# Kernel tuning notes

Hardware: AMD Instinct MI355X
Metric: run time of the kernel (lower is better)

Reference implementation:

```python
import jax, jax.numpy as jnp
import numpy as np

B, L, T = 16, 256, 256
ENC, DEC, MEL, SPK = 256, 1024, 80, 256
ATT, FILT, K = 128, 32, 31


def setup_inputs() -> dict:
    key = jax.random.key(0)
    ks = jax.random.split(key, 32)
    s = 0.05
    r = lambda k, shape: jax.random.normal(k, shape, dtype=jnp.float32) * s
    return {
        'encoder_outputs': jax.random.normal(ks[0], (B, L, ENC), dtype=jnp.float32),
        'speaker_embed': jax.random.normal(ks[1], (B, SPK), dtype=jnp.float32),
        'mels': jax.random.normal(ks[2], (B, T, MEL), dtype=jnp.float32),
        # prenet
        'W_pre1': r(ks[3], (DEC, MEL)), 'b_pre1': jnp.zeros((DEC,), jnp.float32),
        'W_pre2': r(ks[4], (DEC, DEC)), 'b_pre2': jnp.zeros((DEC,), jnp.float32),
        # speaker projection
        'W_sp': r(ks[5], (DEC, SPK)), 'b_sp': jnp.zeros((DEC,), jnp.float32),
        # location-sensitive attention (Tacotron-2 style)
        'W_q': r(ks[6], (ATT, DEC)),
        'W_m': r(ks[7], (ATT, ENC)),
        'W_loc_conv': r(ks[8], (FILT, 2, K)),
        'W_loc': r(ks[9], (ATT, FILT)),
        'v_att': r(ks[10], (ATT,)),
        # LSTM cells
        'W_ih1': r(ks[11], (4 * DEC, DEC + ENC)), 'W_hh1': r(ks[12], (4 * DEC, DEC)),
        'b_ih1': jnp.zeros((4 * DEC,), jnp.float32), 'b_hh1': jnp.zeros((4 * DEC,), jnp.float32),
        'W_ih2': r(ks[13], (4 * DEC, DEC)), 'W_hh2': r(ks[14], (4 * DEC, DEC)),
        'b_ih2': jnp.zeros((4 * DEC,), jnp.float32), 'b_hh2': jnp.zeros((4 * DEC,), jnp.float32),
        # output projections
        'W_mel': r(ks[15], (MEL, DEC)), 'b_mel': jnp.zeros((MEL,), jnp.float32),
        'W_stop': r(ks[16], (1, DEC)), 'b_stop': jnp.zeros((1,), jnp.float32),
    }


def _lstm_cell(x, h, c, W_ih, W_hh, b_ih, b_hh):
    g = x @ W_ih.T + h @ W_hh.T + b_ih + b_hh
    i, f, gg, o = jnp.split(g, 4, axis=-1)
    c2 = jax.nn.sigmoid(f) * c + jax.nn.sigmoid(i) * jnp.tanh(gg)
    h2 = jax.nn.sigmoid(o) * jnp.tanh(c2)
    return h2, c2


def reference(encoder_outputs, speaker_embed, mels,
              W_pre1, b_pre1, W_pre2, b_pre2, W_sp, b_sp,
              W_q, W_m, W_loc_conv, W_loc, v_att,
              W_ih1, W_hh1, b_ih1, b_hh1, W_ih2, W_hh2, b_ih2, b_hh2,
              W_mel, b_mel, W_stop, b_stop):
    b = encoder_outputs.shape[0]
    proc_mem = jnp.einsum('bld,ad->bla', encoder_outputs, W_m)  # [B,L,ATT]
    spk = speaker_embed @ W_sp.T + b_sp                          # [B,DEC]
    # teacher forcing: step 0 uses zeros, step i>0 uses mels[:, i] (matches torch loop)
    prev_mel_seq = jnp.concatenate([jnp.zeros_like(mels[:, :1]), mels[:, 1:]], axis=1)
    prev_mel_seq = prev_mel_seq.transpose(1, 0, 2)               # [T,B,MEL]

    def step(carry, prev_mel):
        h1, c1, h2, c2, prev_w, cum_w = carry
        # prenet (dropout = identity in eval)
        p = jax.nn.relu(prev_mel @ W_pre1.T + b_pre1)
        p = jax.nn.relu(p @ W_pre2.T + b_pre2)
        q = p + spk
        # location features over [prev, cumulative] attention weights
        loc = jnp.stack([prev_w, cum_w], axis=1)                 # [B,2,L]
        f = jax.lax.conv_general_dilated(loc, W_loc_conv, (1,), [(K // 2, K // 2)],
                                         dimension_numbers=('NCH', 'OIH', 'NCH'))  # [B,FILT,L]
        e = jnp.einsum('bla,a->bl', jnp.tanh((q @ W_q.T)[:, None, :]
                                             + jnp.einsum('bcl,ac->bla', f, W_loc)
                                             + proc_mem), v_att)  # [B,L]
        w = jax.nn.softmax(e, axis=1)
        ctx = jnp.einsum('bl,bld->bd', w, encoder_outputs)        # [B,ENC]
        h1n, c1n = _lstm_cell(jnp.concatenate([p, ctx], axis=1), h1, c1, W_ih1, W_hh1, b_ih1, b_hh1)
        h2n, c2n = _lstm_cell(h1n, h2, c2, W_ih2, W_hh2, b_ih2, b_hh2)
        mel = h2n @ W_mel.T + b_mel
        stop = jax.nn.sigmoid(h2n @ W_stop.T + b_stop)
        return (h1n, c1n, h2n, c2n, w, cum_w + w), (mel, stop)

    z = lambda d: jnp.zeros((b, d), jnp.float32)
    carry0 = (z(DEC), z(DEC), z(DEC), z(DEC), z(L), z(L))
    _, (mel_seq, stop_seq) = jax.lax.scan(step, carry0, prev_mel_seq)
    return mel_seq.transpose(1, 0, 2), stop_seq.transpose(1, 0, 2)
```

## Files before the change

kernel.cpp:

```cpp
#include <hip/hip_runtime.h>


namespace {

constexpr int TT = 256, BB = 16, LL = 256, MELD = 80, FILTD = 32, KC = 31;
constexpr int P1 = 2308;
constexpr int P2 = 2052;

typedef float f32x4 __attribute__((ext_vector_type(4)));

struct Args {
  const float *enc, *spe, *mels;
  const float *Wpre1, *bpre1, *Wpre2, *bpre2, *Wsp, *bsp;
  const float *Wq, *Wm, *Wconv, *Wloc, *vatt;
  const float *Wih1, *Whh1, *bih1, *bhh1;
  const float *Wih2, *Whh2, *bih2, *bhh2;
  const float *Wmel, *bmel, *Wstop, *bstop;
  float *p, *X, *qp2, *pm2, *prevmel;
  float *h1a, *h1b, *c1, *h2a, *h2b, *c2;
  float *cum, *wexp, *uctx, *pctx, *psum, *spkvec, *spkq;
  float *W81, *b81, *tmp;
  int *slots, *epoch, *pslots, *pepoch;
  float *out;
};

__device__ __forceinline__ float fast_tanh(float x) {
  float ax = fabsf(x);
  float e = __expf(-2.f * ax);
  float t = (1.f - e) / (1.f + e);
  return copysignf(t, x);
}
__device__ __forceinline__ float fast_sig(float x) { return 1.f / (1.f + __expf(-x)); }

__device__ __forceinline__ float cld1(const float* p) {
  float v;
  asm volatile("global_load_dword %0, %1, off sc0 sc1\n\ts_waitcnt vmcnt(0)"
               : "=v"(v) : "v"(p) : "memory");
  return v;
}
__device__ __forceinline__ int cldi(const int* p) {
  int v;
  asm volatile("global_load_dword %0, %1, off sc0 sc1\n\ts_waitcnt vmcnt(0)"
               : "=v"(v) : "v"(p) : "memory");
  return v;
}
__device__ __forceinline__ void cst1(float* p, float v) {
  asm volatile("global_store_dword %0, %1, off sc0 sc1" :: "v"(p), "v"(v) : "memory");
}
__device__ __forceinline__ void csti(int* p, int v) {
  asm volatile("global_store_dword %0, %1, off sc0 sc1" :: "v"(p), "v"(v) : "memory");
}
__device__ __forceinline__ void cld4(f32x4 d[4], const f32x4* q0, const f32x4* q1,
                                     const f32x4* q2, const f32x4* q3) {
  asm volatile(
      "global_load_dwordx4 %0, %4, off sc0 sc1\n\t"
      "global_load_dwordx4 %1, %5, off sc0 sc1\n\t"
      "global_load_dwordx4 %2, %6, off sc0 sc1\n\t"
      "global_load_dwordx4 %3, %7, off sc0 sc1\n\t"
      "s_waitcnt vmcnt(0)"
      : "=&v"(d[0]), "=&v"(d[1]), "=&v"(d[2]), "=&v"(d[3])
      : "v"(q0), "v"(q1), "v"(q2), "v"(q3)
      : "memory");
}
__device__ __forceinline__ void cld8(f32x4 d[8], const f32x4* q0, const f32x4* q1,
                                     const f32x4* q2, const f32x4* q3, const f32x4* q4,
                                     const f32x4* q5, const f32x4* q6, const f32x4* q7) {
  asm volatile(
      "global_load_dwordx4 %0, %8, off sc0 sc1\n\t"
      "global_load_dwordx4 %1, %9, off sc0 sc1\n\t"
      "global_load_dwordx4 %2, %10, off sc0 sc1\n\t"
      "global_load_dwordx4 %3, %11, off sc0 sc1\n\t"
      "global_load_dwordx4 %4, %12, off sc0 sc1\n\t"
      "global_load_dwordx4 %5, %13, off sc0 sc1\n\t"
      "global_load_dwordx4 %6, %14, off sc0 sc1\n\t"
      "global_load_dwordx4 %7, %15, off sc0 sc1\n\t"
      "s_waitcnt vmcnt(0)"
      : "=&v"(d[0]), "=&v"(d[1]), "=&v"(d[2]), "=&v"(d[3]),
        "=&v"(d[4]), "=&v"(d[5]), "=&v"(d[6]), "=&v"(d[7])
      : "v"(q0), "v"(q1), "v"(q2), "v"(q3), "v"(q4), "v"(q5), "v"(q6), "v"(q7)
      : "memory");
}
__device__ __forceinline__ void cld8d(float d[8], const float* q0, const float* q1,
                                      const float* q2, const float* q3, const float* q4,
                                      const float* q5, const float* q6, const float* q7) {
  asm volatile(
      "global_load_dword %0, %8, off sc0 sc1\n\t"
      "global_load_dword %1, %9, off sc0 sc1\n\t"
      "global_load_dword %2, %10, off sc0 sc1\n\t"
      "global_load_dword %3, %11, off sc0 sc1\n\t"
      "global_load_dword %4, %12, off sc0 sc1\n\t"
      "global_load_dword %5, %13, off sc0 sc1\n\t"
      "global_load_dword %6, %14, off sc0 sc1\n\t"
      "global_load_dword %7, %15, off sc0 sc1\n\t"
      "s_waitcnt vmcnt(0)"
      : "=&v"(d[0]), "=&v"(d[1]), "=&v"(d[2]), "=&v"(d[3]),
        "=&v"(d[4]), "=&v"(d[5]), "=&v"(d[6]), "=&v"(d[7])
      : "v"(q0), "v"(q1), "v"(q2), "v"(q3), "v"(q4), "v"(q5), "v"(q6), "v"(q7)
      : "memory");
}

__device__ __forceinline__ void gridbar(int* slots, int* epoch, int target) {
  __syncthreads();
  if (blockIdx.x == 0) {
    if (threadIdx.x == 0) csti(&slots[0], target);
    while (cldi(&slots[threadIdx.x * 32]) < target) __builtin_amdgcn_s_sleep(1);
    __syncthreads();
    if (threadIdx.x == 0) csti(epoch, target);
  } else {
    if (threadIdx.x == 0) {
      csti(&slots[blockIdx.x * 32], target);
      while (cldi(epoch) < target) __builtin_amdgcn_s_sleep(8);
    }
  }
  __syncthreads();
}

__global__ void k_init(float* base, int n) {
  int i = blockIdx.x * blockDim.x + threadIdx.x;
  if (i < n) base[i] = 0.f;
}

__global__ void k_setpsum(float* psum) {
  if (threadIdx.x < 16) psum[256 + threadIdx.x * 16] = 1.f;
}

__global__ void k_prevmel(Args a) {
  int i = blockIdx.x * blockDim.x + threadIdx.x;
  if (i >= TT * BB * MELD) return;
  int m = i % MELD;
  int tb = i / MELD;
  int b = tb & 15, t = tb >> 4;
  a.prevmel[i] = (t == 0) ? 0.f : a.mels[(b * TT + t) * MELD + m];
}

__global__ void k_spkvec(Args a) {
  int i = blockIdx.x * blockDim.x + threadIdx.x;
  if (i >= BB * 1024) return;
  int b = i >> 10, j = i & 1023;
  const float* x = a.spe + b * 256;
  const float* w = a.Wsp + j * 256;
  float s = a.bsp[j];
  for (int k = 0; k < 256; ++k) s += x[k] * w[k];
  a.spkvec[i] = s;
}

__global__ void k_spkq(Args a) {
  int i = blockIdx.x * blockDim.x + threadIdx.x;
  if (i >= BB * 128) return;
  int b = i >> 7, q = i & 127;
  const float* x = a.spkvec + b * 1024;
  const float* w = a.Wq + q * 1024;
  float s = 0.f;
  for (int k = 0; k < 1024; ++k) s += x[k] * w[k];
  a.spkq[i] = s;
}

__global__ void k_prep81(Args a) {
  int i = blockIdx.x * blockDim.x + threadIdx.x;
  if (i < 81 * 1024) {
    int r = i >> 10, k = i & 1023;
    a.W81[i] = (r < 80) ? a.Wmel[r * 1024 + k] : a.Wstop[k];
  }
  if (i < 81) a.b81[i] = (i < 80) ? a.bmel[i] : a.bstop[0];
}

__global__ __launch_bounds__(256) void k_gemm(const float* __restrict__ A,
                                              const float* __restrict__ Bm,
                                              const float* __restrict__ bias,
                                              float* __restrict__ C,
                                              int M, int N, int K, int act) {
  __shared__ __align__(16) float As[16][132];
  __shared__ __align__(16) float Bs[16][68];
  const int bm = blockIdx.y * 128, bn = blockIdx.x * 64;
  const int tid = threadIdx.x;
  const int tm = (tid >> 4) * 8, tn = (tid & 15) * 4;
  float acc[8][4] = {};
  for (int k0 = 0; k0 < K; k0 += 16) {
    for (int i = tid; i < 512; i += 256) {
      int m = i >> 2, kq = i & 3;
      float4 v = *(const float4*)(A + (size_t)(bm + m) * K + k0 + kq * 4);
      As[kq * 4 + 0][m] = v.x; As[kq * 4 + 1][m] = v.y;
      As[kq * 4 + 2][m] = v.z; As[kq * 4 + 3][m] = v.w;
    }
    {
      int m = tid >> 2, kq = tid & 3;
      float4 v = *(const float4*)(Bm + (size_t)(bn + m) * K + k0 + kq * 4);
      Bs[kq * 4 + 0][m] = v.x; Bs[kq * 4 + 1][m] = v.y;
      Bs[kq * 4 + 2][m] = v.z; Bs[kq * 4 + 3][m] = v.w;
    }
    __syncthreads();
#pragma unroll
    for (int kk = 0; kk < 16; ++kk) {
      float4 a0 = *(const float4*)&As[kk][tm];
      float4 a1 = *(const float4*)&As[kk][tm + 4];
      float4 b0 = *(const float4*)&Bs[kk][tn];
      float av[8] = {a0.x, a0.y, a0.z, a0.w, a1.x, a1.y, a1.z, a1.w};
      float bv[4] = {b0.x, b0.y, b0.z, b0.w};
#pragma unroll
      for (int i = 0; i < 8; ++i)
#pragma unroll
        for (int j = 0; j < 4; ++j) acc[i][j] += av[i] * bv[j];
    }
    __syncthreads();
  }
#pragma unroll
  for (int i = 0; i < 8; ++i)
#pragma unroll
    for (int j = 0; j < 4; ++j) {
      float v = acc[i][j];
      if (bias) v += bias[bn + tn + j];
      if (act == 1) v = fmaxf(v, 0.f);
      C[(size_t)(bm + tm + i) * N + bn + tn + j] = v;
    }
}

__global__ void k_pm_transpose(Args a) {
  int i = blockIdx.x * blockDim.x + threadIdx.x;
  if (i >= BB * 128 * LL) return;
  int l = i & 255;
  int rest = i >> 8;
  int q = rest & 127, b = rest >> 7;
  a.pm2[i] = a.X[(size_t)((b << 8) + l) * 128 + q];
}

__global__ void k_addspkq(Args a) {
  int i = blockIdx.x * blockDim.x + threadIdx.x;
  if (i >= TT * BB * 128) return;
  int q = i & 127, b = (i >> 7) & 15;
  a.qp2[i] += a.spkq[b * 128 + q];
}

__global__ __launch_bounds__(256, 1) void k_barprobe(Args a) {
  for (int t = 0; t < 512; ++t) gridbar(a.pslots, a.pepoch, t + 1);
}

__global__ __launch_bounds__(256, 1) void k_persist(Args a) {
  __shared__ __align__(16) float xs[16 * P1];
  __shared__ float gbuf[16][20];
  const int wg = blockIdx.x, tid = threadIdx.x;
  const int wv = tid >> 6, lane = tid & 63;
  const int d0 = wg * 4, kl = lane * 4;

  float4 wL1[9][4];
  float4 wL2[8][4];
#pragma unroll
  for (int q = 0; q < 4; ++q) {
    const int row = wv * 1024 + d0 + q;
    const float* rih1 = a.Wih1 + (size_t)row * 1280;
    const float* rhh1 = a.Whh1 + (size_t)row * 1024;
    const float* rih2 = a.Wih2 + (size_t)row * 1024;
    const float* rhh2 = a.Whh2 + (size_t)row * 1024;
#pragma unroll
    for (int kb = 0; kb < 9; ++kb)
      wL1[kb][q] = (kb < 5) ? *(const float4*)(rih1 + kb * 256 + kl)
                            : *(const float4*)(rhh1 + kb * 256 + kl - 1280);
#pragma unroll
    for (int kb = 0; kb < 8; ++kb)
      wL2[kb][q] = (kb < 4) ? *(const float4*)(rih2 + kb * 256 + kl)
                            : *(const float4*)(rhh2 + kb * 256 + kl - 1024);
  }
  const int row_r = wv * 1024 + d0 + (lane >> 4);
  const float bsum1 = a.bih1[row_r] + a.bhh1[row_r];
  const float bsum2 = a.bih2[row_r] + a.bhh2[row_r];

  for (int t = 0; t < 259; ++t) {
    const int cur = t & 1, prv = cur ^ 1;

    if (t < 256) {
      float* loc0 = xs;
      float* loc1 = xs + 64;
      float* F = xs + 128;
      float* expv = xs + 672;
      const int b = wg >> 4, c = wg & 15, l0 = c << 4;
      float sm;
      {
        const f32x4* ps4 = (const f32x4*)(a.psum + prv * 256 + b * 16);
        f32x4 pd[4];
        cld4(pd, ps4, ps4 + 1, ps4 + 2, ps4 + 3);
        sm = 0.f;
#pragma unroll
        for (int i = 0; i < 4; ++i) sm += pd[i][0] + pd[i][1] + pd[i][2] + pd[i][3];
      }
      const float inv_ps = 1.f / sm;
      if (tid < 64) {
        int lp = l0 - 16 + tid;
        bool ok = (lp >= 0 && lp < LL);
        float we = 0.f, cm = 0.f;
        if (ok) {
          we = cld1(a.wexp + prv * 4096 + b * 256 + lp) * inv_ps;
          cm = cld1(a.cum + prv * 4096 + b * 256 + lp);
        }
        loc0[tid] = we;
        loc1[tid] = ok ? (cm + we) : 0.f;
      }
      __syncthreads();
      if (tid < 16) cst1(a.cum + cur * 4096 + b * 256 + l0 + tid, loc1[16 + tid]);
      for (int idx = tid; idx < FILTD * 16; idx += 256) {
        int fc = idx >> 4, ll = idx & 15;
        const float* w = a.Wconv + fc * 62;
        float s = 0.f;
#pragma unroll
        for (int k = 0; k < KC; ++k) {
          s += w[k] * loc0[ll + k + 1];
          s += w[31 + k] * loc1[ll + k + 1];
        }
        F[fc * 17 + ll] = s;
      }
      __syncthreads();
      {
        const int ll = tid >> 4, ag = tid & 15;
        const int l = l0 + ll;
        const float* qpb = a.qp2 + (size_t)((t << 4) + b) * 128;
        const float* pmb = a.pm2 + (size_t)b * 128 * 256;
        float s = 0.f;
        for (int q = ag * 8; q < ag * 8 + 8; ++q) {
          float x = qpb[q] + pmb[q * 256 + l];
          const float* wl = a.Wloc + q * 32;
#pragma unroll
          for (int fc = 0; fc < FILTD; ++fc) x += wl[fc] * F[fc * 17 + ll];
          s += a.vatt[q] * fast_tanh(x);
        }
        s += __shfl_down(s, 8, 16);
        s += __shfl_down(s, 4, 16);
        s += __shfl_down(s, 2, 16);
        s += __shfl_down(s, 1, 16);
        if (ag == 0) {
          float ex = __expf(s);
          expv[ll] = ex;
          cst1(a.wexp + cur * 4096 + b * 256 + l, ex);
        }
      }
      __syncthreads();
      if (tid == 0) {
        float s = 0.f;
#pragma unroll
        for (int i = 0; i < 16; ++i) s += expv[i];
        cst1(a.psum + cur * 256 + b * 16 + c, s);
      }
      {
        float s = 0.f;
        const float* eb = a.enc + (size_t)((b << 8) + l0) * 256 + tid;
#pragma unroll
        for (int ll = 0; ll < 16; ++ll) s += expv[ll] * eb[ll * 256];
        cst1(a.pctx + cur * 65536 + (b * 16 + c) * 256 + tid, s);
      }
      __syncthreads();
    }

    if (wg < 16 && t >= 1 && t <= 256) {
      const int s = t - 1, par = s & 1, b = wg;
      float sm;
      {
        const f32x4* ps4 = (const f32x4*)(a.psum + par * 256 + b * 16);
        f32x4 pd[4];
        cld4(pd, ps4, ps4 + 1, ps4 + 2, ps4 + 3);
        sm = 0.f;
#pragma unroll
        for (int i = 0; i < 4; ++i) sm += pd[i][0] + pd[i][1] + pd[i][2] + pd[i][3];
      }
      const float inv = 1.f / sm;
      const float* pc = a.pctx + par * 65536 + b * 4096 + tid;
      float d[8];
      float acc = 0.f;
      cld8d(d, pc, pc + 256, pc + 512, pc + 768, pc + 1024, pc + 1280, pc + 1536,
            pc + 1792);
#pragma unroll
      for (int i = 0; i < 8; ++i) acc += d[i];
      cld8d(d, pc + 2048, pc + 2304, pc + 2560, pc + 2816, pc + 3072, pc + 3328,
            pc + 3584, pc + 3840);
#pragma unroll
      for (int i = 0; i < 8; ++i) acc += d[i];
      cst1(a.uctx + par * 4096 + b * 256 + tid, acc * inv);
    }

    if (t >= 2 && t <= 257) {
      const int s1 = t - 2;
      const float* pt = a.p + (size_t)s1 * 16384;
      const float* h1r = (s1 & 1) ? a.h1a : a.h1b;
      float* h1w = (s1 & 1) ? a.h1b : a.h1a;
      for (int k = 0; k < 16; ++k) {
        int i4 = tid + k * 256, b = i4 >> 8, kq = i4 & 255;
        *(f32x4*)(xs + b * P1 + kq * 4) = *(const f32x4*)(pt + (size_t)i4 * 4);
      }
      {
        const f32x4* q = (const f32x4*)(a.uctx + (size_t)(s1 & 1) * 4096);
        f32x4 d[4];
        cld4(d, q + tid, q + tid + 256, q + tid + 512, q + tid + 768);
#pragma unroll
        for (int k = 0; k < 4; ++k) {
          int i4 = tid + k * 256, b = i4 >> 6, kq = i4 & 63;
          *(f32x4*)(xs + b * P1 + 1024 + kq * 4) = d[k];
        }
      }
      {
        const f32x4* q = (const f32x4*)h1r;
        f32x4 d[8];
#pragma unroll
        for (int hb = 0; hb < 2; ++hb) {
          const f32x4* qq = q + tid + hb * 2048;
          cld8(d, qq, qq + 256, qq + 512, qq + 768, qq + 1024, qq + 1280, qq + 1536,
               qq + 1792);
#pragma unroll
          for (int k = 0; k < 8; ++k) {
            int i4 = tid + (hb * 8 + k) * 256, b = i4 >> 8, kq = i4 & 255;
            *(f32x4*)(xs + b * P1 + 1280 + kq * 4) = d[k];
          }
        }
      }
      __syncthreads();
      float acc[4][16];
#pragma unroll
      for (int q = 0; q < 4; ++q)
#pragma unroll
        for (int b = 0; b < 16; ++b) acc[q][b] = 0.f;
#pragma unroll
      for (int kb = 0; kb < 9; ++kb) {
        const float* xb = xs + kb * 256 + kl;
#pragma unroll
        for (int b = 0; b < 16; ++b) {
          float4 x4 = *(const float4*)(xb + b * P1);
#pragma unroll
          for (int q = 0; q < 4; ++q) {
            acc[q][b] += wL1[kb][q].x * x4.x;
            acc[q][b] += wL1[kb][q].y * x4.y;
            acc[q][b] += wL1[kb][q].z * x4.z;
            acc[q][b] += wL1[kb][q].w * x4.w;
          }
        }
      }
      __syncthreads();
      float* red = xs + wv * 4352;
#pragma unroll
      for (int q = 0; q < 4; ++q)
#pragma unroll
        for (int b = 0; b < 16; ++b) red[(q * 16 + b) * 68 + lane] = acc[q][b];
      __syncthreads();
      {
        const float* rr = xs + wv * 4352 + lane * 68;
        float4 s4 = {0.f, 0.f, 0.f, 0.f};
#pragma unroll
        for (int i = 0; i < 16; ++i) {
          float4 v = *(const float4*)(rr + i * 4);
          s4.x += v.x; s4.y += v.y; s4.z += v.z; s4.w += v.w;
        }
        gbuf[wv * 4 + (lane >> 4)][lane & 15] = s4.x + s4.y + s4.z + s4.w + bsum1;
      }
      __syncthreads();
      if (tid < 64) {
        int dd = tid >> 4, b = tid & 15;
        int d = d0 + dd;
        float gi = gbuf[0 + dd][b], gf = gbuf[4 + dd][b];
        float gg = gbuf[8 + dd][b], go = gbuf[12 + dd][b];
        float co = a.c1[b * 1024 + d];
        float cn = fast_sig(gf) * co + fast_sig(gi) * fast_tanh(gg);
        float hn = fast_sig(go) * fast_tanh(cn);
        a.c1[b * 1024 + d] = cn;
        cst1(h1w + b * 1024 + d, hn);
      }
      __syncthreads();
    }

    if (t >= 3) {
      const int s2 = t - 3;
      const float* h1s = (s2 & 1) ? a.h1b : a.h1a;
      const float* h2r = (s2 & 1) ? a.h2a : a.h2b;
      float* h2w = (s2 & 1) ? a.h2b : a.h2a;
      {
        f32x4 d[8];
        const f32x4* q1 = (const f32x4*)h1s;
        const f32x4* q2 = (const f32x4*)h2r;
#pragma unroll
        for (int hb = 0; hb < 2; ++hb) {
          const f32x4* qq = q1 + tid + hb * 2048;
          cld8(d, qq, qq + 256, qq + 512, qq + 768, qq + 1024, qq + 1280, qq + 1536,
               qq + 1792);
#pragma unroll
          for (int k = 0; k < 8; ++k) {
            int i4 = tid + (hb * 8 + k) * 256, b = i4 >> 8, kq = i4 & 255;
            *(f32x4*)(xs + b * P2 + kq * 4) = d[k];
          }
        }
#pragma unroll
        for (int hb = 0; hb < 2; ++hb) {
          const f32x4* qq = q2 + tid + hb * 2048;
          cld8(d, qq, qq + 256, qq + 512, qq + 768, qq + 1024, qq + 1280, qq + 1536,
               qq + 1792);
#pragma unroll
          for (int k = 0; k < 8; ++k) {
            int i4 = tid + (hb * 8 + k) * 256, b = i4 >> 8, kq = i4 & 255;
            *(f32x4*)(xs + b * P2 + 1024 + kq * 4) = d[k];
          }
        }
      }
      __syncthreads();
      float acc[4][16];
#pragma unroll
      for (int q = 0; q < 4; ++q)
#pragma unroll
        for (int b = 0; b < 16; ++b) acc[q][b] = 0.f;
#pragma unroll
      for (int kb = 0; kb < 8; ++kb) {
        const float* xb = xs + kb * 256 + kl;
#pragma unroll
        for (int b = 0; b < 16; ++b) {
          float4 x4 = *(const float4*)(xb + b * P2);
#pragma unroll
          for (int q = 0; q < 4; ++q) {
            acc[q][b] += wL2[kb][q].x * x4.x;
            acc[q][b] += wL2[kb][q].y * x4.y;
            acc[q][b] += wL2[kb][q].z * x4.z;
            acc[q][b] += wL2[kb][q].w * x4.w;
          }
        }
      }
      __syncthreads();
      float* red = xs + wv * 4352;
#pragma unroll
      for (int q = 0; q < 4; ++q)
#pragma unroll
        for (int b = 0; b < 16; ++b) red[(q * 16 + b) * 68 + lane] = acc[q][b];
      __syncthreads();
      {
        const float* rr = xs + wv * 4352 + lane * 68;
        float4 s4 = {0.f, 0.f, 0.f, 0.f};
#pragma unroll
        for (int i = 0; i < 16; ++i) {
          float4 v = *(const float4*)(rr + i * 4);
          s4.x += v.x; s4.y += v.y; s4.z += v.z; s4.w += v.w;
        }
        gbuf[wv * 4 + (lane >> 4)][lane & 15] = s4.x + s4.y + s4.z + s4.w + bsum2;
      }
      __syncthreads();
      if (tid < 64) {
        int dd = tid >> 4, b = tid & 15;
        int d = d0 + dd;
        float gi = gbuf[0 + dd][b], gf = gbuf[4 + dd][b];
        float gg = gbuf[8 + dd][b], go = gbuf[12 + dd][b];
        float co = a.c2[b * 1024 + d];
        float cn = fast_sig(gf) * co + fast_sig(gi) * fast_tanh(gg);
        float hn = fast_sig(go) * fast_tanh(cn);
        a.c2[b * 1024 + d] = cn;
        cst1(h2w + b * 1024 + d, hn);
        a.X[(size_t)(s2 * 16 + b) * 1024 + d] = hn;
      }
    }

    if (t < 258) gridbar(a.slots, a.epoch, t + 1);
  }
}

__global__ void k_finish(Args a) {
  int i = blockIdx.x * blockDim.x + threadIdx.x;
  if (i >= 4096 * 128) return;
  int col = i & 127, tb = i >> 7;
  int t = tb >> 4, b = tb & 15;
  float v = a.tmp[i];
  if (col < 80) a.out[(size_t)(b * 256 + t) * 80 + col] = v;
  else if (col == 80) a.out[327680 + b * 256 + t] = fast_sig(v);
}

}

extern "C" void kernel_launch(void* const* d_in, const int* in_sizes, int n_in,
                              void* d_out, int out_size, void* d_ws, size_t ws_size,
                              hipStream_t stream) {
  float* ws = (float*)d_ws;
  Args a;
  a.enc = (const float*)d_in[0];
  a.spe = (const float*)d_in[1];
  a.mels = (const float*)d_in[2];
  a.Wpre1 = (const float*)d_in[3];  a.bpre1 = (const float*)d_in[4];
  a.Wpre2 = (const float*)d_in[5];  a.bpre2 = (const float*)d_in[6];
  a.Wsp = (const float*)d_in[7];    a.bsp = (const float*)d_in[8];
  a.Wq = (const float*)d_in[9];     a.Wm = (const float*)d_in[10];
  a.Wconv = (const float*)d_in[11]; a.Wloc = (const float*)d_in[12];
  a.vatt = (const float*)d_in[13];
  a.Wih1 = (const float*)d_in[14];  a.Whh1 = (const float*)d_in[15];
  a.bih1 = (const float*)d_in[16];  a.bhh1 = (const float*)d_in[17];
  a.Wih2 = (const float*)d_in[18];  a.Whh2 = (const float*)d_in[19];
  a.bih2 = (const float*)d_in[20];  a.bhh2 = (const float*)d_in[21];
  a.Wmel = (const float*)d_in[22];  a.bmel = (const float*)d_in[23];
  a.Wstop = (const float*)d_in[24]; a.bstop = (const float*)d_in[25];

  a.p    = ws + 0;
  a.X    = ws + 4194304;
  a.qp2  = ws + 8388608;
  a.pm2  = ws + 8912896;
  float* st = ws + 9437184;
  a.h1a = st + 0;      a.h1b = st + 16384;
  a.c1  = st + 32768;
  a.h2a = st + 49152;  a.h2b = st + 65536;
  a.c2  = st + 81920;
  a.cum  = st + 98304;
  a.wexp = st + 106496;
  a.uctx = st + 114688;
  a.pctx = st + 122880;
  a.psum = st + 253952;
  a.slots  = (int*)(st + 254464);
  a.epoch  = (int*)(st + 262656);
  a.pslots = (int*)(st + 262688);
  a.pepoch = (int*)(st + 270880);
  a.spkvec = ws + 9708096;
  a.spkq   = ws + 9724480;
  a.W81    = ws + 9726528;
  a.b81    = ws + 9857600;
  a.tmp    = ws + 9857728;
  a.prevmel = a.tmp;
  a.out = (float*)d_out;

  k_init<<<(270912 + 255) / 256, 256, 0, stream>>>(st, 270912);
  k_setpsum<<<1, 64, 0, stream>>>(a.psum);
  k_prevmel<<<(TT * BB * MELD + 255) / 256, 256, 0, stream>>>(a);
  k_spkvec<<<(BB * 1024 + 255) / 256, 256, 0, stream>>>(a);
  k_spkq<<<(BB * 128 + 255) / 256, 256, 0, stream>>>(a);
  k_prep81<<<(81 * 1024 + 255) / 256, 256, 0, stream>>>(a);

  k_gemm<<<dim3(16, 32), 256, 0, stream>>>(a.prevmel, a.Wpre1, a.bpre1, a.X, 4096, 1024, 80, 1);
  k_gemm<<<dim3(16, 32), 256, 0, stream>>>(a.X, a.Wpre2, a.bpre2, a.p, 4096, 1024, 1024, 1);
  k_gemm<<<dim3(2, 32), 256, 0, stream>>>(a.p, a.Wq, nullptr, a.qp2, 4096, 128, 1024, 0);
  k_addspkq<<<(TT * BB * 128 + 255) / 256, 256, 0, stream>>>(a);
  k_gemm<<<dim3(2, 32), 256, 0, stream>>>(a.enc, a.Wm, nullptr, a.X, 4096, 128, 256, 0);
  k_pm_transpose<<<(BB * 128 * LL + 255) / 256, 256, 0, stream>>>(a);

  {
    void* kargs[] = {(void*)&a};
    hipError_t e = hipLaunchCooperativeKernel(reinterpret_cast<const void*>(&k_barprobe),
                                              dim3(256), dim3(256), kargs, 0, stream);
    if (e != hipSuccess) k_barprobe<<<256, 256, 0, stream>>>(a);
  }

  {
    void* kargs[] = {(void*)&a};
    hipError_t e = hipLaunchCooperativeKernel(reinterpret_cast<const void*>(&k_persist),
                                              dim3(256), dim3(256), kargs, 0, stream);
    if (e != hipSuccess) k_persist<<<256, 256, 0, stream>>>(a);
  }

  k_gemm<<<dim3(2, 32), 256, 0, stream>>>(a.X, a.W81, a.b81, a.tmp, 4096, 128, 1024, 0);
  k_finish<<<(4096 * 128 + 255) / 256, 256, 0, stream>>>(a);
}
```

Before: 14.00 ms.

## Drop barrier probe kernel, use acquire fence instead of coherent loads, keep cell state in registers

Removes the k_barprobe warm-up kernel, which ran 512 grid barriers before the persistent kernel on every call. The inline-asm coherent loads (sc0 sc1 with vmcnt(0) waits) become ordinary cached loads, and an agent-scope acquire fence after each grid barrier supplies cross-block visibility. The LSTM cell states c1 and c2 now stay in per-thread registers instead of making a global round trip each step. This lets the compiler batch and overlap loads, at the risk of stale data if the fence semantics don't cover all cached reads.

```diff
diff --git a/kernel.cpp b/kernel.cpp
--- a/kernel.cpp
+++ b/kernel.cpp
@@ -32,12 +32,6 @@
 }
 __device__ __forceinline__ float fast_sig(float x) { return 1.f / (1.f + __expf(-x)); }
 
-__device__ __forceinline__ float cld1(const float* p) {
-  float v;
-  asm volatile("global_load_dword %0, %1, off sc0 sc1\n\ts_waitcnt vmcnt(0)"
-               : "=v"(v) : "v"(p) : "memory");
-  return v;
-}
 __device__ __forceinline__ int cldi(const int* p) {
   int v;
   asm volatile("global_load_dword %0, %1, off sc0 sc1\n\ts_waitcnt vmcnt(0)"
@@ -49,54 +43,6 @@
 }
 __device__ __forceinline__ void csti(int* p, int v) {
   asm volatile("global_store_dword %0, %1, off sc0 sc1" :: "v"(p), "v"(v) : "memory");
-}
-__device__ __forceinline__ void cld4(f32x4 d[4], const f32x4* q0, const f32x4* q1,
-                                     const f32x4* q2, const f32x4* q3) {
-  asm volatile(
-      "global_load_dwordx4 %0, %4, off sc0 sc1\n\t"
-      "global_load_dwordx4 %1, %5, off sc0 sc1\n\t"
-      "global_load_dwordx4 %2, %6, off sc0 sc1\n\t"
-      "global_load_dwordx4 %3, %7, off sc0 sc1\n\t"
-      "s_waitcnt vmcnt(0)"
-      : "=&v"(d[0]), "=&v"(d[1]), "=&v"(d[2]), "=&v"(d[3])
-      : "v"(q0), "v"(q1), "v"(q2), "v"(q3)
-      : "memory");
-}
-__device__ __forceinline__ void cld8(f32x4 d[8], const f32x4* q0, const f32x4* q1,
-                                     const f32x4* q2, const f32x4* q3, const f32x4* q4,
-                                     const f32x4* q5, const f32x4* q6, const f32x4* q7) {
-  asm volatile(
-      "global_load_dwordx4 %0, %8, off sc0 sc1\n\t"
-      "global_load_dwordx4 %1, %9, off sc0 sc1\n\t"
-      "global_load_dwordx4 %2, %10, off sc0 sc1\n\t"
-      "global_load_dwordx4 %3, %11, off sc0 sc1\n\t"
-      "global_load_dwordx4 %4, %12, off sc0 sc1\n\t"
-      "global_load_dwordx4 %5, %13, off sc0 sc1\n\t"
-      "global_load_dwordx4 %6, %14, off sc0 sc1\n\t"
-      "global_load_dwordx4 %7, %15, off sc0 sc1\n\t"
-      "s_waitcnt vmcnt(0)"
-      : "=&v"(d[0]), "=&v"(d[1]), "=&v"(d[2]), "=&v"(d[3]),
-        "=&v"(d[4]), "=&v"(d[5]), "=&v"(d[6]), "=&v"(d[7])
-      : "v"(q0), "v"(q1), "v"(q2), "v"(q3), "v"(q4), "v"(q5), "v"(q6), "v"(q7)
-      : "memory");
-}
-__device__ __forceinline__ void cld8d(float d[8], const float* q0, const float* q1,
-                                      const float* q2, const float* q3, const float* q4,
-                                      const float* q5, const float* q6, const float* q7) {
-  asm volatile(
-      "global_load_dword %0, %8, off sc0 sc1\n\t"
-      "global_load_dword %1, %9, off sc0 sc1\n\t"
-      "global_load_dword %2, %10, off sc0 sc1\n\t"
-      "global_load_dword %3, %11, off sc0 sc1\n\t"
-      "global_load_dword %4, %12, off sc0 sc1\n\t"
-      "global_load_dword %5, %13, off sc0 sc1\n\t"
-      "global_load_dword %6, %14, off sc0 sc1\n\t"
-      "global_load_dword %7, %15, off sc0 sc1\n\t"
-      "s_waitcnt vmcnt(0)"
-      : "=&v"(d[0]), "=&v"(d[1]), "=&v"(d[2]), "=&v"(d[3]),
-        "=&v"(d[4]), "=&v"(d[5]), "=&v"(d[6]), "=&v"(d[7])
-      : "v"(q0), "v"(q1), "v"(q2), "v"(q3), "v"(q4), "v"(q5), "v"(q6), "v"(q7)
-      : "memory");
 }
 
 __device__ __forceinline__ void gridbar(int* slots, int* epoch, int target) {
@@ -112,6 +58,7 @@
       while (cldi(epoch) < target) __builtin_amdgcn_s_sleep(8);
     }
   }
+  __builtin_amdgcn_fence(__ATOMIC_ACQUIRE, "agent");
   __syncthreads();
 }
 
@@ -230,10 +177,6 @@
   a.qp2[i] += a.spkq[b * 128 + q];
 }
 
-__global__ __launch_bounds__(256, 1) void k_barprobe(Args a) {
-  for (int t = 0; t < 512; ++t) gridbar(a.pslots, a.pepoch, t + 1);
-}
-
 __global__ __launch_bounds__(256, 1) void k_persist(Args a) {
   __shared__ __align__(16) float xs[16 * P1];
   __shared__ float gbuf[16][20];
@@ -263,6 +206,8 @@
   const float bsum1 = a.bih1[row_r] + a.bhh1[row_r];
   const float bsum2 = a.bih2[row_r] + a.bhh2[row_r];
 
+  float c1v = 0.f, c2v = 0.f;
+
   for (int t = 0; t < 259; ++t) {
     const int cur = t & 1, prv = cur ^ 1;
 
@@ -272,14 +217,14 @@
       float* F = xs + 128;
       float* expv = xs + 672;
       const int b = wg >> 4, c = wg & 15, l0 = c << 4;
-      float sm;
+      float sm = 0.f;
       {
         const f32x4* ps4 = (const f32x4*)(a.psum + prv * 256 + b * 16);
-        f32x4 pd[4];
-        cld4(pd, ps4, ps4 + 1, ps4 + 2, ps4 + 3);
-        sm = 0.f;
-#pragma unroll
-        for (int i = 0; i < 4; ++i) sm += pd[i][0] + pd[i][1] + pd[i][2] + pd[i][3];
+#pragma unroll
+        for (int i = 0; i < 4; ++i) {
+          f32x4 v = ps4[i];
+          sm += v[0] + v[1] + v[2] + v[3];
+        }
       }
       const float inv_ps = 1.f / sm;
       if (tid < 64) {
@@ -287,8 +232,8 @@
         bool ok = (lp >= 0 && lp < LL);
         float we = 0.f, cm = 0.f;
         if (ok) {
-          we = cld1(a.wexp + prv * 4096 + b * 256 + lp) * inv_ps;
-          cm = cld1(a.cum + prv * 4096 + b * 256 + lp);
+          we = a.wexp[prv * 4096 + b * 256 + lp] * inv_ps;
+          cm = a.cum[prv * 4096 + b * 256 + lp];
         }
         loc0[tid] = we;
         loc1[tid] = ok ? (cm + we) : 0.f;
@@ -349,27 +294,20 @@
 
     if (wg < 16 && t >= 1 && t <= 256) {
       const int s = t - 1, par = s & 1, b = wg;
-      float sm;
+      float sm = 0.f;
       {
         const f32x4* ps4 = (const f32x4*)(a.psum + par * 256 + b * 16);
-        f32x4 pd[4];
-        cld4(pd, ps4, ps4 + 1, ps4 + 2, ps4 + 3);
-        sm = 0.f;
-#pragma unroll
-        for (int i = 0; i < 4; ++i) sm += pd[i][0] + pd[i][1] + pd[i][2] + pd[i][3];
+#pragma unroll
+        for (int i = 0; i < 4; ++i) {
+          f32x4 v = ps4[i];
+          sm += v[0] + v[1] + v[2] + v[3];
+        }
       }
       const float inv = 1.f / sm;
       const float* pc = a.pctx + par * 65536 + b * 4096 + tid;
-      float d[8];
       float acc = 0.f;
-      cld8d(d, pc, pc + 256, pc + 512, pc + 768, pc + 1024, pc + 1280, pc + 1536,
-            pc + 1792);
-#pragma unroll
-      for (int i = 0; i < 8; ++i) acc += d[i];
-      cld8d(d, pc + 2048, pc + 2304, pc + 2560, pc + 2816, pc + 3072, pc + 3328,
-            pc + 3584, pc + 3840);
-#pragma unroll
-      for (int i = 0; i < 8; ++i) acc += d[i];
+#pragma unroll
+      for (int i = 0; i < 16; ++i) acc += pc[i * 256];
       cst1(a.uctx + par * 4096 + b * 256 + tid, acc * inv);
     }
 
@@ -385,7 +323,8 @@
       {
         const f32x4* q = (const f32x4*)(a.uctx + (size_t)(s1 & 1) * 4096);
         f32x4 d[4];
-        cld4(d, q + tid, q + tid + 256, q + tid + 512, q + tid + 768);
+#pragma unroll
+        for (int k = 0; k < 4; ++k) d[k] = q[tid + k * 256];
 #pragma unroll
         for (int k = 0; k < 4; ++k) {
           int i4 = tid + k * 256, b = i4 >> 6, kq = i4 & 63;
@@ -394,12 +333,12 @@
       }
       {
         const f32x4* q = (const f32x4*)h1r;
-        f32x4 d[8];
 #pragma unroll
         for (int hb = 0; hb < 2; ++hb) {
+          f32x4 d[8];
           const f32x4* qq = q + tid + hb * 2048;
-          cld8(d, qq, qq + 256, qq + 512, qq + 768, qq + 1024, qq + 1280, qq + 1536,
-               qq + 1792);
+#pragma unroll
+          for (int k = 0; k < 8; ++k) d[k] = qq[k * 256];
 #pragma unroll
           for (int k = 0; k < 8; ++k) {
             int i4 = tid + (hb * 8 + k) * 256, b = i4 >> 8, kq = i4 & 255;
@@ -451,10 +390,10 @@
         int d = d0 + dd;
         float gi = gbuf[0 + dd][b], gf = gbuf[4 + dd][b];
         float gg = gbuf[8 + dd][b], go = gbuf[12 + dd][b];
-        float co = a.c1[b * 1024 + d];
+        float co = c1v;
         float cn = fast_sig(gf) * co + fast_sig(gi) * fast_tanh(gg);
         float hn = fast_sig(go) * fast_tanh(cn);
-        a.c1[b * 1024 + d] = cn;
+        c1v = cn;
         cst1(h1w + b * 1024 + d, hn);
       }
       __syncthreads();
@@ -466,14 +405,14 @@
       const float* h2r = (s2 & 1) ? a.h2a : a.h2b;
       float* h2w = (s2 & 1) ? a.h2b : a.h2a;
       {
-        f32x4 d[8];
         const f32x4* q1 = (const f32x4*)h1s;
         const f32x4* q2 = (const f32x4*)h2r;
 #pragma unroll
         for (int hb = 0; hb < 2; ++hb) {
+          f32x4 d[8];
           const f32x4* qq = q1 + tid + hb * 2048;
-          cld8(d, qq, qq + 256, qq + 512, qq + 768, qq + 1024, qq + 1280, qq + 1536,
-               qq + 1792);
+#pragma unroll
+          for (int k = 0; k < 8; ++k) d[k] = qq[k * 256];
 #pragma unroll
           for (int k = 0; k < 8; ++k) {
             int i4 = tid + (hb * 8 + k) * 256, b = i4 >> 8, kq = i4 & 255;
@@ -482,9 +421,10 @@
         }
 #pragma unroll
         for (int hb = 0; hb < 2; ++hb) {
+          f32x4 d[8];
           const f32x4* qq = q2 + tid + hb * 2048;
-          cld8(d, qq, qq + 256, qq + 512, qq + 768, qq + 1024, qq + 1280, qq + 1536,
-               qq + 1792);
+#pragma unroll
+          for (int k = 0; k < 8; ++k) d[k] = qq[k * 256];
 #pragma unroll
           for (int k = 0; k < 8; ++k) {
             int i4 = tid + (hb * 8 + k) * 256, b = i4 >> 8, kq = i4 & 255;
@@ -536,12 +476,12 @@
         int d = d0 + dd;
         float gi = gbuf[0 + dd][b], gf = gbuf[4 + dd][b];
         float gg = gbuf[8 + dd][b], go = gbuf[12 + dd][b];
-        float co = a.c2[b * 1024 + d];
+        float co = c2v;
         float cn = fast_sig(gf) * co + fast_sig(gi) * fast_tanh(gg);
         float hn = fast_sig(go) * fast_tanh(cn);
-        a.c2[b * 1024 + d] = cn;
+        c2v = cn;
         cst1(h2w + b * 1024 + d, hn);
-        a.X[(size_t)(s2 * 16 + b) * 1024 + d] = hn;
+        cst1(&a.X[(size_t)(s2 * 16 + b) * 1024 + d], hn);
       }
     }
 
@@ -624,13 +564,6 @@
 
   {
     void* kargs[] = {(void*)&a};
-    hipError_t e = hipLaunchCooperativeKernel(reinterpret_cast<const void*>(&k_barprobe),
-                                              dim3(256), dim3(256), kargs, 0, stream);
-    if (e != hipSuccess) k_barprobe<<<256, 256, 0, stream>>>(a);
-  }
-
-  {
-    void* kargs[] = {(void*)&a};
     hipError_t e = hipLaunchCooperativeKernel(reinterpret_cast<const void*>(&k_persist),
                                               dim3(256), dim3(256), kargs, 0, stream);
     if (e != hipSuccess) k_persist<<<256, 256, 0, stream>>>(a);
```

New measurement: 14.74 ms. 1.05x slower.
